# Kernel tuning notes

Measured on AMD Instinct MI355X. Metric: run time of the kernel, lower is better.

Reference implementation:

```python
import jax, jax.numpy as jnp
import numpy as np

EPS = 1e-6          # numerical floor for norms / denominators (fp32-safe)
PROJ_EPS = 1e-5     # ball projection margin: max norm = 1 - PROJ_EPS


def _norm(x):
    return jnp.sqrt(jnp.maximum(jnp.sum(x * x, axis=-1, keepdims=True), EPS * EPS))


def hyp_proj(x):
    # project onto open Poincare ball of radius 1 - PROJ_EPS
    n = _norm(x)
    scale = jnp.minimum((1.0 - PROJ_EPS) / n, 1.0)
    return x * scale


def exp_map_zero(v):
    n = _norm(v)
    return jnp.tanh(n) * v / n


def log_map_zero(y):
    n = _norm(y)
    return jnp.arctanh(jnp.minimum(n, 1.0 - PROJ_EPS)) * y / n


def mobius_add(x, y):
    x2 = jnp.sum(x * x, axis=-1, keepdims=True)
    y2 = jnp.sum(y * y, axis=-1, keepdims=True)
    xy = jnp.sum(x * y, axis=-1, keepdims=True)
    num = (1.0 + 2.0 * xy + y2) * x + (1.0 - x2) * y
    den = 1.0 + 2.0 * xy + x2 * y2
    return num / jnp.maximum(den, EPS)


def gcn_layer(x, rows, cols, vals, W, b, n_nodes, use_act):
    # tangent-space linear transform
    pre = log_map_zero(x)                      # [N, d]
    h = pre @ W                                # [N, d]
    # sparse adjacency matmul: agg[r] += val * h[c]
    msg = vals[:, None] * h[cols]              # [E, d]
    agg = jax.ops.segment_sum(msg, rows, num_segments=n_nodes)
    out = hyp_proj(exp_map_zero(agg))
    # hyperbolic bias via mobius addition
    bh = hyp_proj(exp_map_zero(b[None, :]))    # [1, d]
    out = hyp_proj(mobius_add(out, bh))
    if use_act:
        out = hyp_proj(exp_map_zero(jnp.tanh(log_map_zero(out))))
    return out


def setup_inputs() -> dict:
    key = jax.random.key(0)
    N, D, E = 100000, 64, 3200000
    ks = jax.random.split(key, 8)
    x = jax.random.normal(ks[0], (N, D), dtype=jnp.float32) * 0.1
    edge_vals = jax.random.uniform(ks[1], (E,), dtype=jnp.float32)
    W1 = jax.random.normal(ks[2], (D, D), dtype=jnp.float32) * (1.0 / np.sqrt(D))
    b1 = jnp.zeros((D,), dtype=jnp.float32)
    W2 = jax.random.normal(ks[3], (D, D), dtype=jnp.float32) * (1.0 / np.sqrt(D))
    b2 = jnp.zeros((D,), dtype=jnp.float32)
    edge_rows = jax.random.randint(ks[4], (E,), 0, N, dtype=jnp.int64 if jax.config.jax_enable_x64 else jnp.int32).astype(jnp.int32)
    edge_cols = jax.random.randint(ks[5], (E,), 0, N, dtype=jnp.int32)
    return {"x": x, "edge_vals": edge_vals, "W1": W1, "b1": b1,
            "W2": W2, "b2": b2, "edge_rows": edge_rows, "edge_cols": edge_cols}


def reference(x, edge_vals, W1, b1, W2, b2, edge_rows, edge_cols):
    n_nodes = x.shape[0]
    # HyperKA._graph_convolution: project base embeddings, then layers with
    # mobius residual; last layer has no activation.
    e0 = hyp_proj(x)
    h1 = gcn_layer(e0, edge_rows, edge_cols, edge_vals, W1, b1, n_nodes, use_act=True)
    h1 = hyp_proj(mobius_add(h1, e0))
    h2 = gcn_layer(h1, edge_rows, edge_cols, edge_vals, W2, b2, n_nodes, use_act=False)
    h2 = hyp_proj(mobius_add(h2, h1))
    return h2
```

## Files before the change

### kernel.cpp

```cpp
#include <hip/hip_runtime.h>
#include <math.h>

#define D 64
#define EPSF 1e-6f
#define EPS2F 1e-12f
#define PROJ_EPSF 1e-5f
#define EPB 16384

typedef _Float16 f16;
typedef f16 f16x4 __attribute__((ext_vector_type(4)));
typedef f16 f16x8 __attribute__((ext_vector_type(8)));
typedef float f32x4 __attribute__((ext_vector_type(4)));

__device__ __forceinline__ float frcp(float x)  { return __builtin_amdgcn_rcpf(x); }
__device__ __forceinline__ float fsqrt(float x) { return __builtin_amdgcn_sqrtf(x); }
__device__ __forceinline__ float ftanh(float x) {
    float e = __expf(2.0f * x);
    return (e - 1.0f) * frcp(e + 1.0f);
}
__device__ __forceinline__ float fatanh(float z) {
    return 0.5f * __logf((1.0f + z) * frcp(1.0f - z));
}

__device__ __forceinline__ float wave_sum(float v) {
#pragma unroll
    for (int o = 32; o > 0; o >>= 1) v += __shfl_xor(v, o, 64);
    return v;
}
__device__ __forceinline__ float qsum(float v) {
#pragma unroll
    for (int o = 1; o < 16; o <<= 1) v += __shfl_xor(v, o, 64);
    return v;
}

__global__ __launch_bounds__(256) void k1_hist_pre(
    const int* __restrict__ rows, const float* __restrict__ x,
    const float* __restrict__ b1, const float* __restrict__ b2,
    int* __restrict__ histT, f16* __restrict__ pre,
    float* __restrict__ nbuf, float* __restrict__ bhbuf,
    int E, int N, int nb1, int NBIN)
{
    const int bid = blockIdx.x, tid = threadIdx.x;
    const int lane = tid & 63;
    if (bid < nb1) {
        __shared__ int lh[512];
        for (int i = tid; i < NBIN; i += 256) lh[i] = 0;
        __syncthreads();
        const int e0 = bid * EPB;
#pragma unroll 4
        for (int k = 0; k < EPB / 256; ++k) {
            int e = e0 + k * 256 + tid;
            if (e < E) atomicAdd(&lh[__builtin_nontemporal_load(rows + e) >> 8], 1);
        }
        __syncthreads();
        for (int i = tid; i < NBIN; i += 256) histT[i * nb1 + bid] = lh[i];
    } else if (bid == nb1) {
        if (tid < 128) {
            int wsel = tid >> 6;
            const float* b = wsel ? b2 : b1;
            float bv = b[lane];
            float nb = fsqrt(fmaxf(wave_sum(bv * bv), EPS2F));
            float t = ftanh(nb);
            float v = bv * (t * frcp(nb));
            float nv = t;
            float sc = fminf((1.0f - PROJ_EPSF) * frcp(fmaxf(nv, EPSF)), 1.0f);
            v *= sc; nv = fminf(nv, 1.0f - PROJ_EPSF);
            bhbuf[wsel * 64 + lane] = v;
            if (lane == 0) bhbuf[128 + wsel] = nv;
        }
    } else {
        int node = (bid - nb1 - 1) * 4 + (tid >> 6);
        if (node >= N) return;
        float xv = x[(size_t)node * D + lane];
        float nx = fsqrt(fmaxf(wave_sum(xv * xv), EPS2F));
        float sc = fminf((1.0f - PROJ_EPSF) * frcp(nx), 1.0f);
        float e0 = xv * sc;
        float ne0 = fminf(nx, 1.0f - PROJ_EPSF);
        pre[(size_t)node * D + lane] = (f16)(e0 * (fatanh(ne0) * frcp(fmaxf(ne0, EPSF))));
        if (lane == 0) nbuf[node] = nx;
    }
}

__global__ __launch_bounds__(64) void scan_parts(int* __restrict__ part, int P)
{
    int lane = threadIdx.x;
    int carry = 0;
    for (int b = 0; b < P; b += 64) {
        int i = b + lane;
        int v = (i < P) ? part[i] : 0;
        int inc = v;
#pragma unroll
        for (int off = 1; off < 64; off <<= 1) {
            int tu = __shfl_up(inc, off, 64);
            if (lane >= off) inc += tu;
        }
        if (i < P) part[i] = inc - v + carry;
        carry += __shfl(inc, 63, 64);
    }
}

__global__ __launch_bounds__(256) void scan_apply(
    int* __restrict__ a, const int* __restrict__ part, int L)
{
    __shared__ int wbase[4];
    int t = threadIdx.x, lane = t & 63, wid = t >> 6;
    int idx0 = blockIdx.x * 1024 + t * 4;
    int v0 = 0, v1 = 0, v2 = 0, v3 = 0;
    if (idx0 < L) { int4 v = *(const int4*)(a + idx0); v0 = v.x; v1 = v.y; v2 = v.z; v3 = v.w; }
    int s = v0 + v1 + v2 + v3;
    int inc = s;
#pragma unroll
    for (int off = 1; off < 64; off <<= 1) {
        int tu = __shfl_up(inc, off, 64);
        if (lane >= off) inc += tu;
    }
    if (lane == 63) wbase[wid] = inc;
    __syncthreads();
    if (t == 0) { int acc = 0; for (int k = 0; k < 4; ++k) { int xx = wbase[k]; wbase[k] = acc; acc += xx; } }
    __syncthreads();
    int excl = part[blockIdx.x] + wbase[wid] + (inc - s);
    if (idx0 < L) {
        int4 o; o.x = excl; o.y = excl + v0; o.z = excl + v0 + v1; o.w = excl + v0 + v1 + v2;
        *(int4*)(a + idx0) = o;
    }
}

__device__ __forceinline__ void gemm64_body(
    const f16* __restrict__ A, const float* __restrict__ W,
    f16* __restrict__ C, int M, int wid, int nwaves, int lane)
{
    const int m = lane & 15;
    const int quad = lane >> 4;
    f16x8 Bfr[2][4];
#pragma unroll
    for (int kt = 0; kt < 2; ++kt)
#pragma unroll
        for (int nt = 0; nt < 4; ++nt) {
            f16x8 tmp;
#pragma unroll
            for (int j = 0; j < 8; ++j)
                tmp[j] = (f16)W[(kt * 32 + quad * 8 + j) * D + nt * 16 + m];
            Bfr[kt][nt] = tmp;
        }
    const int ntile = M >> 4;
    for (int tile = wid; tile < ntile; tile += nwaves) {
        const f16* arow = A + (size_t)(tile * 16 + m) * D;
        f16x8 a0 = *(const f16x8*)(arow + quad * 8);
        f16x8 a1 = *(const f16x8*)(arow + 32 + quad * 8);
#pragma unroll
        for (int nt = 0; nt < 4; ++nt) {
            f32x4 z = {0.0f, 0.0f, 0.0f, 0.0f};
            z = __builtin_amdgcn_mfma_f32_16x16x32_f16(a0, Bfr[0][nt], z, 0, 0, 0);
            z = __builtin_amdgcn_mfma_f32_16x16x32_f16(a1, Bfr[1][nt], z, 0, 0, 0);
#pragma unroll
            for (int r = 0; r < 4; ++r)
                C[(size_t)(tile * 16 + quad * 4 + r) * D + nt * 16 + m] = (f16)z[r];
        }
    }
}

__global__ __launch_bounds__(256) void k2_reduce_gemm(
    const int* __restrict__ histT, int* __restrict__ part, int Lp, int P,
    const f16* __restrict__ A, const float* __restrict__ W,
    f16* __restrict__ C, int M)
{
    const int tid = threadIdx.x, lane = tid & 63, wid4 = tid >> 6;
    if ((int)blockIdx.x < P) {
        __shared__ int ws[4];
        int idx0 = blockIdx.x * 1024 + tid * 4;
        int s = 0;
        if (idx0 < Lp) { int4 v = *(const int4*)(histT + idx0); s = v.x + v.y + v.z + v.w; }
        s = (int)wave_sum((float)s);
        if (lane == 0) ws[wid4] = s;
        __syncthreads();
        if (tid == 0) part[blockIdx.x] = ws[0] + ws[1] + ws[2] + ws[3];
    } else {
        int wid = (blockIdx.x - P) * 4 + wid4;
        int nwaves = (gridDim.x - P) * 4;
        gemm64_body(A, W, C, M, wid, nwaves, lane);
    }
}

__global__ __launch_bounds__(256) void gemm64(
    const f16* __restrict__ A, const float* __restrict__ W,
    f16* __restrict__ C, int M)
{
    gemm64_body(A, W, C, M, blockIdx.x * 4 + (threadIdx.x >> 6), gridDim.x * 4,
                threadIdx.x & 63);
}

__global__ __launch_bounds__(256) void p1_scatter(
    const int* __restrict__ rows, const int* __restrict__ cols,
    const float* __restrict__ vals, const int* __restrict__ histT,
    unsigned int* __restrict__ pay, unsigned char* __restrict__ rloc,
    int E, int nb1, int NBIN)
{
    __shared__ int cur[512];
    const int bid = blockIdx.x, tid = threadIdx.x;
    for (int i = tid; i < NBIN; i += 256) cur[i] = histT[i * nb1 + bid];
    __syncthreads();
    const int e0 = bid * EPB;
#pragma unroll 4
    for (int k = 0; k < EPB / 256; ++k) {
        int e = e0 + k * 256 + tid;
        if (e < E) {
            int r = __builtin_nontemporal_load(rows + e);
            int c = __builtin_nontemporal_load(cols + e);
            float v = __builtin_nontemporal_load(vals + e);
            unsigned int q = (unsigned int)fmaf(v, 32767.0f, 0.5f);
            unsigned int p = (q << 17) | (unsigned int)c;
            int pos = atomicAdd(&cur[r >> 8], 1);
            pay[pos] = p;
            rloc[pos] = (unsigned char)(r & 255);
        }
    }
}

__global__ __launch_bounds__(256) void band_build(
    const unsigned int* __restrict__ pay, const unsigned char* __restrict__ rloc,
    const int* __restrict__ histT, int* __restrict__ rs,
    unsigned int* __restrict__ epack, int E, int nb1, int NBIN, int N)
{
    __shared__ int lh[256];
    __shared__ int cur[256];
    __shared__ int wsum[4];
    const int b = blockIdx.x, tid = threadIdx.x;
    const int lane = tid & 63, wid = tid >> 6;
    const int segstart = histT[b * nb1];
    const int segend = (b + 1 < NBIN) ? histT[(b + 1) * nb1] : E;
    lh[tid] = 0;
    __syncthreads();
    for (int j = segstart + tid; j < segend; j += 256)
        atomicAdd(&lh[rloc[j]], 1);
    __syncthreads();
    int v = lh[tid];
    int inc = v;
#pragma unroll
    for (int off = 1; off < 64; off <<= 1) {
        int tu = __shfl_up(inc, off, 64);
        if (lane >= off) inc += tu;
    }
    if (lane == 63) wsum[wid] = inc;
    __syncthreads();
    int base = 0;
    for (int w2 = 0; w2 < wid; ++w2) base += wsum[w2];
    int excl = base + inc - v;
    cur[tid] = excl;
    int r = b * 256 + tid;
    if (r < N) rs[r] = segstart + excl + v;
    __syncthreads();
    for (int j = segstart + tid; j < segend; j += 256) {
        int pos = segstart + atomicAdd(&cur[rloc[j]], 1);
        epack[pos] = pay[j];
    }
}

__device__ __forceinline__ void csr_accum4(
    const int* __restrict__ rs, const unsigned int* __restrict__ epack,
    const f16* __restrict__ h, int row, int li, int qbase, float* a)
{
    const int start = (row == 0) ? 0 : rs[row - 1];
    const int end = rs[row];
    int nbat = (end - start + 15) >> 4;
#pragma unroll
    for (int o = 16; o < 64; o <<= 1) {
        int nbo = __shfl_xor(nbat, o, 64);
        nbat = nbo > nbat ? nbo : nbat;
    }
    const f16x4* __restrict__ h4 = (const f16x4*)h;
    float A0[4] = {0.f, 0.f, 0.f, 0.f}, A1[4] = {0.f, 0.f, 0.f, 0.f};
    for (int bb = 0; bb < nbat; ++bb) {
        int j = start + bb * 16 + li;
        unsigned int p = (j < end) ? epack[j] : 0u;
        int c = (int)(p & 131071u);
        float vf = (float)(p >> 17) * (1.0f / 32767.0f);
#pragma unroll
        for (int t = 0; t < 16; t += 2) {
            int   c0 = __shfl(c, qbase + t, 64);
            float v0 = __shfl(vf, qbase + t, 64);
            int   c1 = __shfl(c, qbase + t + 1, 64);
            float v1 = __shfl(vf, qbase + t + 1, 64);
            f16x4 h0 = h4[(size_t)c0 * 16 + li];
            f16x4 h1 = h4[(size_t)c1 * 16 + li];
#pragma unroll
            for (int k = 0; k < 4; ++k) {
                A0[k] = fmaf(v0, (float)h0[k], A0[k]);
                A1[k] = fmaf(v1, (float)h1[k], A1[k]);
            }
        }
    }
#pragma unroll
    for (int k = 0; k < 4; ++k) a[k] = A0[k] + A1[k];
}

__global__ __launch_bounds__(256) void layer1_fused(
    const int* __restrict__ rs, const unsigned int* __restrict__ epack,
    const f16* __restrict__ h, const float* __restrict__ x,
    const float* __restrict__ bhbuf, float* __restrict__ nbuf,
    f16* __restrict__ h1_out, f16* __restrict__ pre2_out, int N)
{
    const int lane = threadIdx.x & 63;
    const int q = lane >> 4, li = lane & 15, qbase = q << 4;
    int row = blockIdx.x * 16 + (threadIdx.x >> 6) * 4 + q;
    if (row >= N) row = N - 1;

    float a[4];
    csr_accum4(rs, epack, h, row, li, qbase, a);

    float na = fsqrt(fmaxf(qsum(a[0]*a[0] + a[1]*a[1] + a[2]*a[2] + a[3]*a[3]), EPS2F));
    float t = ftanh(na);
    float s = t * frcp(na);
    float o[4];
#pragma unroll
    for (int k = 0; k < 4; ++k) o[k] = a[k] * s;
    float no = t;
    float sc = fminf((1.0f - PROJ_EPSF) * frcp(fmaxf(no, EPSF)), 1.0f);
#pragma unroll
    for (int k = 0; k < 4; ++k) o[k] *= sc;
    no = fminf(no, 1.0f - PROJ_EPSF);

    float4 bp4 = ((const float4*)bhbuf)[li];
    float bh[4] = {bp4.x, bp4.y, bp4.z, bp4.w};
    float nbh = bhbuf[128];
    float xy = qsum(o[0]*bh[0] + o[1]*bh[1] + o[2]*bh[2] + o[3]*bh[3]);
    float x2 = no * no, y2 = nbh * nbh;
    float rd = frcp(fmaxf(1.0f + 2.0f * xy + x2 * y2, EPSF));
    float al = (1.0f + 2.0f * xy + y2) * rd;
    float be = (1.0f - x2) * rd;
    float m[4];
#pragma unroll
    for (int k = 0; k < 4; ++k) m[k] = al * o[k] + be * bh[k];
    float nm = fsqrt(fmaxf(al*al*x2 + be*be*y2 + 2.0f*al*be*xy, EPS2F));
    sc = fminf((1.0f - PROJ_EPSF) * frcp(fmaxf(nm, EPSF)), 1.0f);
#pragma unroll
    for (int k = 0; k < 4; ++k) m[k] *= sc;
    nm = fminf(nm, 1.0f - PROJ_EPSF);

    float lg = fatanh(nm) * frcp(fmaxf(nm, EPSF));
    float w[4];
#pragma unroll
    for (int k = 0; k < 4; ++k) w[k] = ftanh(m[k] * lg);
    float nw = fsqrt(fmaxf(qsum(w[0]*w[0] + w[1]*w[1] + w[2]*w[2] + w[3]*w[3]), EPS2F));
    float tw = ftanh(nw);
    s = tw * frcp(nw);
    float ov[4];
#pragma unroll
    for (int k = 0; k < 4; ++k) ov[k] = w[k] * s;
    float nov = tw;
    sc = fminf((1.0f - PROJ_EPSF) * frcp(fmaxf(nov, EPSF)), 1.0f);
#pragma unroll
    for (int k = 0; k < 4; ++k) ov[k] *= sc;
    nov = fminf(nov, 1.0f - PROJ_EPSF);

    float4 xp4 = ((const float4*)(x + (size_t)row * D))[li];
    float xp[4] = {xp4.x, xp4.y, xp4.z, xp4.w};
    float nx = nbuf[row];
    float sce = fminf((1.0f - PROJ_EPSF) * frcp(nx), 1.0f);
    float e0[4];
#pragma unroll
    for (int k = 0; k < 4; ++k) e0[k] = xp[k] * sce;
    float ne0 = fminf(nx, 1.0f - PROJ_EPSF);
    float xy2 = qsum(ov[0]*e0[0] + ov[1]*e0[1] + ov[2]*e0[2] + ov[3]*e0[3]);
    x2 = nov * nov; y2 = ne0 * ne0;
    rd = frcp(fmaxf(1.0f + 2.0f * xy2 + x2 * y2, EPSF));
    al = (1.0f + 2.0f * xy2 + y2) * rd;
    be = (1.0f - x2) * rd;
    float h1v[4];
#pragma unroll
    for (int k = 0; k < 4; ++k) h1v[k] = al * ov[k] + be * e0[k];
    float nh = fsqrt(fmaxf(al*al*x2 + be*be*y2 + 2.0f*al*be*xy2, EPS2F));
    sc = fminf((1.0f - PROJ_EPSF) * frcp(fmaxf(nh, EPSF)), 1.0f);
#pragma unroll
    for (int k = 0; k < 4; ++k) h1v[k] *= sc;
    nh = fminf(nh, 1.0f - PROJ_EPSF);

    f16x4 hp, pp;
    float lg2 = fatanh(nh) * frcp(fmaxf(nh, EPSF));
#pragma unroll
    for (int k = 0; k < 4; ++k) { hp[k] = (f16)h1v[k]; pp[k] = (f16)(h1v[k] * lg2); }
    ((f16x4*)h1_out)[(size_t)row * 16 + li] = hp;
    ((f16x4*)pre2_out)[(size_t)row * 16 + li] = pp;
    if (li == 0) nbuf[row] = nh;
}

__global__ __launch_bounds__(256) void layer2_fused(
    const int* __restrict__ rs, const unsigned int* __restrict__ epack,
    const f16* __restrict__ h2lin, const float* __restrict__ bhbuf,
    const float* __restrict__ nbuf, f16* __restrict__ h1_inout, int N)
{
    const int lane = threadIdx.x & 63;
    const int q = lane >> 4, li = lane & 15, qbase = q << 4;
    int row = blockIdx.x * 16 + (threadIdx.x >> 6) * 4 + q;
    if (row >= N) row = N - 1;

    float a[4];
    csr_accum4(rs, epack, h2lin, row, li, qbase, a);

    float na = fsqrt(fmaxf(qsum(a[0]*a[0] + a[1]*a[1] + a[2]*a[2] + a[3]*a[3]), EPS2F));
    float t = ftanh(na);
    float s = t * frcp(na);
    float o[4];
#pragma unroll
    for (int k = 0; k < 4; ++k) o[k] = a[k] * s;
    float no = t;
    float sc = fminf((1.0f - PROJ_EPSF) * frcp(fmaxf(no, EPSF)), 1.0f);
#pragma unroll
    for (int k = 0; k < 4; ++k) o[k] *= sc;
    no = fminf(no, 1.0f - PROJ_EPSF);

    float4 bp4 = ((const float4*)(bhbuf + 64))[li];
    float bh[4] = {bp4.x, bp4.y, bp4.z, bp4.w};
    float nbh = bhbuf[129];
    float xy = qsum(o[0]*bh[0] + o[1]*bh[1] + o[2]*bh[2] + o[3]*bh[3]);
    float x2 = no * no, y2 = nbh * nbh;
    float rd = frcp(fmaxf(1.0f + 2.0f * xy + x2 * y2, EPSF));
    float al = (1.0f + 2.0f * xy + y2) * rd;
    float be = (1.0f - x2) * rd;
    float m[4];
#pragma unroll
    for (int k = 0; k < 4; ++k) m[k] = al * o[k] + be * bh[k];
    float nm = fsqrt(fmaxf(al*al*x2 + be*be*y2 + 2.0f*al*be*xy, EPS2F));
    sc = fminf((1.0f - PROJ_EPSF) * frcp(fmaxf(nm, EPSF)), 1.0f);
#pragma unroll
    for (int k = 0; k < 4; ++k) m[k] *= sc;
    nm = fminf(nm, 1.0f - PROJ_EPSF);

    f16x4 hp = ((const f16x4*)h1_inout)[(size_t)row * 16 + li];
    float h1v[4] = {(float)hp[0], (float)hp[1], (float)hp[2], (float)hp[3]};
    float nh = nbuf[row];
    float xy2 = qsum(m[0]*h1v[0] + m[1]*h1v[1] + m[2]*h1v[2] + m[3]*h1v[3]);
    x2 = nm * nm; y2 = nh * nh;
    rd = frcp(fmaxf(1.0f + 2.0f * xy2 + x2 * y2, EPSF));
    al = (1.0f + 2.0f * xy2 + y2) * rd;
    be = (1.0f - x2) * rd;
    float r[4];
#pragma unroll
    for (int k = 0; k < 4; ++k) r[k] = al * m[k] + be * h1v[k];
    float n2 = fsqrt(fmaxf(al*al*x2 + be*be*y2 + 2.0f*al*be*xy2, EPS2F));
    sc = fminf((1.0f - PROJ_EPSF) * frcp(fmaxf(n2, EPSF)), 1.0f);
    f16x4 op;
#pragma unroll
    for (int k = 0; k < 4; ++k) op[k] = (f16)(r[k] * sc);
    ((f16x4*)h1_inout)[(size_t)row * 16 + li] = op;
}

__global__ __launch_bounds__(256) void expand4(
    const f16* __restrict__ src, float* __restrict__ dst, int n4)
{
    int i = blockIdx.x * 256 + threadIdx.x;
    if (i < n4) {
        f16x4 v = ((const f16x4*)src)[i];
        float4 o; o.x = (float)v[0]; o.y = (float)v[1]; o.z = (float)v[2]; o.w = (float)v[3];
        ((float4*)dst)[i] = o;
    }
}

extern "C" void kernel_launch(void* const* d_in, const int* in_sizes, int n_in,
                              void* d_out, int out_size, void* d_ws, size_t ws_size,
                              hipStream_t stream) {
    const float* x    = (const float*)d_in[0];
    const float* vals = (const float*)d_in[1];
    const float* W1   = (const float*)d_in[2];
    const float* b1   = (const float*)d_in[3];
    const float* W2   = (const float*)d_in[4];
    const float* b2   = (const float*)d_in[5];
    const int* rows   = (const int*)d_in[6];
    const int* cols   = (const int*)d_in[7];
    float* out = (float*)d_out;

    const int N = in_sizes[0] / D;
    const int E = in_sizes[1];
    const size_t nd = (size_t)N * D;

    const int NBIN = (N + 255) >> 8;
    const int nb1  = (E + EPB - 1) / EPB;
    const int L    = NBIN * nb1;
    const int Lp   = ((L + 1023) / 1024) * 1024;
    const int P    = Lp / 1024;

    char* w = (char*)d_ws;
    unsigned int*  epack = (unsigned int*)w;
    unsigned int*  pay   = (unsigned int*)(w + (size_t)E * 4);
    f16*           h1    = (f16*)(w + (size_t)E * 4);
    unsigned char* rloc  = (unsigned char*)(w + (size_t)E * 8);
    int*           histT = (int*)(w + (size_t)E * 9);
    size_t off = (size_t)E * 9 + (size_t)Lp * 4;
    int*   part  = (int*)(w + off);            off += 1024;
    int*   rs    = (int*)(w + off);            off += (size_t)N * 4;
    float* nbuf  = (float*)(w + off);          off += (size_t)N * 4;
    float* bhbuf = (float*)(w + off);

    f16* slot0 = (f16*)d_out;
    f16* slot1 = slot0 + nd;

    const int nbpre = (N + 3) / 4;
    const int nbq   = (N + 15) / 16;

    hipMemsetAsync(histT, 0, (size_t)Lp * 4, stream);
    k1_hist_pre<<<nb1 + 1 + nbpre, 256, 0, stream>>>(
        rows, x, b1, b2, histT, slot0, nbuf, bhbuf, E, N, nb1, NBIN);
    k2_reduce_gemm<<<P + 784, 256, 0, stream>>>(histT, part, Lp, P, slot0, W1, slot1, N);
    scan_parts<<<1, 64, 0, stream>>>(part, P);
    scan_apply<<<P, 256, 0, stream>>>(histT, part, Lp);
    p1_scatter<<<nb1, 256, 0, stream>>>(rows, cols, vals, histT, pay, rloc, E, nb1, NBIN);
    band_build<<<NBIN, 256, 0, stream>>>(pay, rloc, histT, rs, epack, E, nb1, NBIN, N);
    layer1_fused<<<nbq, 256, 0, stream>>>(rs, epack, slot1, x, bhbuf, nbuf, h1, slot0, N);
    gemm64<<<784, 256, 0, stream>>>(slot0, W2, slot1, N);
    layer2_fused<<<nbq, 256, 0, stream>>>(rs, epack, slot1, bhbuf, nbuf, h1, N);
    expand4<<<(int)((nd / 4 + 255) / 256), 256, 0, stream>>>(h1, out, (int)(nd / 4));
}
```

Baseline: 403.3 us.

## Stage scatter writes in LDS per bin and flush in 16-element chunks

The partition scatter kernel now buffers each edge's packed payload and row-local byte in per-bin shared-memory staging slots and flushes them to global memory in contiguous 16-entry chunks. This replaces fully random 4-byte and 1-byte global writes with coalesced runs. Overflow entries are still written directly, and the block size grows to 512. It adds about 90KB of LDS per block, which limits occupancy, and the flush loop runs serially per bin thread.

```diff
diff --git a/kernel.cpp b/kernel.cpp
--- a/kernel.cpp
+++ b/kernel.cpp
@@ -189,29 +189,101 @@
                 threadIdx.x & 63);
 }
 
-__global__ __launch_bounds__(256) void p1_scatter(
+__global__ __launch_bounds__(512) void p1_scatter(
     const int* __restrict__ rows, const int* __restrict__ cols,
     const float* __restrict__ vals, const int* __restrict__ histT,
     unsigned int* __restrict__ pay, unsigned char* __restrict__ rloc,
     int E, int nb1, int NBIN)
 {
-    __shared__ int cur[512];
+    __shared__ unsigned int  stage[512][32];
+    __shared__ unsigned char srloc[512][32];
+    __shared__ int gbase[512];
+    __shared__ int cnt[512];
+    __shared__ int flushed[512];
+    __shared__ unsigned int msk[512];
+
     const int bid = blockIdx.x, tid = threadIdx.x;
-    for (int i = tid; i < NBIN; i += 256) cur[i] = histT[i * nb1 + bid];
-    __syncthreads();
+    {
+        int i = tid;
+        gbase[i] = (i < NBIN) ? histT[i * nb1 + bid] : 0;
+        cnt[i] = 0; flushed[i] = 0; msk[i] = 0u;
+    }
+    __syncthreads();
+
     const int e0 = bid * EPB;
-#pragma unroll 4
-    for (int k = 0; k < EPB / 256; ++k) {
-        int e = e0 + k * 256 + tid;
-        if (e < E) {
-            int r = __builtin_nontemporal_load(rows + e);
-            int c = __builtin_nontemporal_load(cols + e);
-            float v = __builtin_nontemporal_load(vals + e);
-            unsigned int q = (unsigned int)fmaf(v, 32767.0f, 0.5f);
-            unsigned int p = (q << 17) | (unsigned int)c;
-            int pos = atomicAdd(&cur[r >> 8], 1);
-            pay[pos] = p;
-            rloc[pos] = (unsigned char)(r & 255);
+    for (int rnd = 0; rnd < EPB / 2048; ++rnd) {
+        int rr[4], cc[4]; float vv[4];
+#pragma unroll
+        for (int u = 0; u < 4; ++u) {
+            int e = e0 + rnd * 2048 + u * 512 + tid;
+            bool ok = e < E;
+            rr[u] = ok ? __builtin_nontemporal_load(rows + e) : -1;
+            cc[u] = ok ? __builtin_nontemporal_load(cols + e) : 0;
+            vv[u] = ok ? __builtin_nontemporal_load(vals + e) : 0.0f;
+        }
+#pragma unroll
+        for (int u = 0; u < 4; ++u) {
+            if (rr[u] < 0) continue;
+            int bin = rr[u] >> 8;
+            unsigned int q = (unsigned int)fmaf(vv[u], 32767.0f, 0.5f);
+            unsigned int p = (q << 17) | (unsigned int)cc[u];
+            unsigned char rl = (unsigned char)(rr[u] & 255);
+            int slot = atomicAdd(&cnt[bin], 1);
+            if (slot - flushed[bin] < 32) {
+                stage[bin][slot & 31] = p;
+                srloc[bin][slot & 31] = rl;
+                atomicOr(&msk[bin], 1u << (slot & 31));
+            } else {
+                int gp = gbase[bin] + slot;
+                pay[gp] = p;
+                rloc[gp] = rl;
+            }
+        }
+        __syncthreads();
+        if (tid < NBIN) {
+            const int b = tid;
+            int f = flushed[b];
+            int n = cnt[b];
+            unsigned int m = msk[b];
+            const int gb = gbase[b];
+            while (n - f >= 16) {
+                const int half = (f >> 4) & 1;
+                const unsigned int m16 = (m >> (half * 16)) & 0xFFFFu;
+                const int base = gb + f;
+                const int r0 = half * 16;
+                if (m16 == 0xFFFFu) {
+#pragma unroll
+                    for (int k2 = 0; k2 < 16; ++k2)
+                        pay[base + k2] = stage[b][r0 + k2];
+#pragma unroll
+                    for (int k2 = 0; k2 < 16; ++k2)
+                        rloc[base + k2] = srloc[b][r0 + k2];
+                } else {
+                    for (int k2 = 0; k2 < 16; ++k2)
+                        if (m16 & (1u << k2)) {
+                            pay[base + k2] = stage[b][r0 + k2];
+                            rloc[base + k2] = srloc[b][r0 + k2];
+                        }
+                }
+                m &= ~(0xFFFFu << (half * 16));
+                f += 16;
+            }
+            flushed[b] = f;
+            msk[b] = m;
+        }
+        __syncthreads();
+    }
+    if (tid < NBIN) {
+        const int b = tid;
+        int f = flushed[b];
+        const int n = cnt[b];
+        const unsigned int m = msk[b];
+        const int gb = gbase[b];
+        for (; f < n; ++f) {
+            if (m & (1u << (f & 31))) {
+                pay[gb + f] = stage[b][f & 31];
+                rloc[gb + f] = srloc[b][f & 31];
+            }
         }
     }
 }
@@ -502,7 +574,7 @@
     k2_reduce_gemm<<<P + 784, 256, 0, stream>>>(histT, part, Lp, P, slot0, W1, slot1, N);
     scan_parts<<<1, 64, 0, stream>>>(part, P);
     scan_apply<<<P, 256, 0, stream>>>(histT, part, Lp);
-    p1_scatter<<<nb1, 256, 0, stream>>>(rows, cols, vals, histT, pay, rloc, E, nb1, NBIN);
+    p1_scatter<<<nb1, 512, 0, stream>>>(rows, cols, vals, histT, pay, rloc, E, nb1, NBIN);
     band_build<<<NBIN, 256, 0, stream>>>(pay, rloc, histT, rs, epack, E, nb1, NBIN, N);
     layer1_fused<<<nbq, 256, 0, stream>>>(rs, epack, slot1, x, bhbuf, nbuf, h1, slot0, N);
     gemm64<<<784, 256, 0, stream>>>(slot0, W2, slot1, N);
```

Result: faster. 352.6 us (-12.6%).
